# Optimization experiments

Hardware: AMD Instinct MI355X
Metric: run time of the kernel (lower is better)

Reference implementation:

```python
import jax, jax.numpy as jnp
import numpy as np

TEMPERATURE = 0.07
NEG_INF = -9e15
EPS = 1e-12

def setup_inputs() -> dict:
    key = jax.random.key(0)
    k1, k2 = jax.random.split(key)
    N, D = 8192, 128
    features = jax.random.normal(k1, (N, D), dtype=jnp.float32)
    labels = jax.random.randint(k2, (N,), 0, 16, dtype=jnp.int64)
    return {"features": features, "labels": labels}

def reference(features, labels):
    N = features.shape[0]
    # L2 normalize rows (torch F.normalize: x / max(||x||, eps))
    norm = jnp.linalg.norm(features, axis=1, keepdims=True)
    f = features / jnp.maximum(norm, EPS)
    # [N, N] similarity
    sim = jnp.matmul(f, f.T) / TEMPERATURE
    eye = jnp.eye(N, dtype=bool)
    sim = jnp.where(eye, NEG_INF, sim)
    # positive-pair mask: same label, excluding self
    pos_mask = ((labels[:, None] == labels[None, :]) & ~eye).astype(sim.dtype)
    denom = jnp.exp(sim).sum(axis=1, keepdims=True)  # [N, 1]
    log_prob = sim - jnp.log(denom + EPS)
    loss = -(pos_mask * log_prob).sum(axis=1) / (pos_mask.sum(axis=1) + EPS)
    return loss.mean()
```

## Files before the change

kernel.cpp:

```cpp
#include <hip/hip_runtime.h>
#include <hip/hip_bf16.h>

#define EPS 1e-12f
#define SQRT_C_EXP 4.53981597f
#define M_LN2F 0.69314718056f
#define NUM_CLASSES 16

#define BM 256
#define BN 128
#define KD 128
#define NCHUNK 8
#define NPART 16
#define PSTRIDE 48

typedef __attribute__((ext_vector_type(4))) float f32x4;
typedef __attribute__((ext_vector_type(8))) short bf16x8;

__device__ __forceinline__ float bf2f(ushort u) {
    unsigned int x = ((unsigned int)u) << 16;
    return __uint_as_float(x);
}

__device__ __forceinline__ const bf16x8* lds_frag(const ushort* base, int r, int slot) {
    int sw = slot ^ (r & 7);
    return reinterpret_cast<const bf16x8*>(
        reinterpret_cast<const char*>(base) + r * 256 + sw * 16);
}

__global__ void normalize_kernel(const float* __restrict__ feat,
                                 ushort* __restrict__ fb,
                                 float* __restrict__ sq,
                                 int N) {
    int r    = (blockIdx.x * blockDim.x + threadIdx.x) >> 6;
    int lane = threadIdx.x & 63;
    if (r >= N) return;
    const float2 v = *reinterpret_cast<const float2*>(feat + (size_t)r * KD + lane * 2);
    float s = v.x * v.x + v.y * v.y;
    #pragma unroll
    for (int off = 1; off < 64; off <<= 1) s += __shfl_xor(s, off);
    const float scale = SQRT_C_EXP / fmaxf(sqrtf(s), EPS);

    __hip_bfloat16 h0 = __float2bfloat16(v.x * scale);
    __hip_bfloat16 h1 = __float2bfloat16(v.y * scale);
    ushort u0 = *reinterpret_cast<ushort*>(&h0);
    ushort u1 = *reinterpret_cast<ushort*>(&h1);
    unsigned int pack = (unsigned int)u0 | ((unsigned int)u1 << 16);
    *reinterpret_cast<unsigned int*>(fb + (size_t)r * KD + lane * 2) = pack;

    float q0 = bf2f(u0), q1 = bf2f(u1);
    float q = q0 * q0 + q1 * q1;
    #pragma unroll
    for (int off = 1; off < 64; off <<= 1) q += __shfl_xor(q, off);
    if (lane == 0) sq[r] = q;
}

__global__ __launch_bounds__(512, 2) void supcon_denom(
    const ushort* __restrict__ fb,
    const int* __restrict__ labels,
    float* __restrict__ part,
    int N) {

    __shared__ __align__(16) ushort As[BM * KD];
    __shared__ __align__(16) ushort Bs[2][BN * KD];

    const int tid  = threadIdx.x;
    const int lane = tid & 63;
    const int w    = tid >> 6;
    const int wr   = w >> 1;
    const int wc   = w & 1;
    const int r16  = lane & 15;
    const int g4   = lane >> 4;

    const int rowbase = blockIdx.y * BM;
    const int col0    = blockIdx.x * (BN * NCHUNK);

    {
        const ushort* gA = fb + (size_t)rowbase * KD;
        #pragma unroll
        for (int i = 0; i < 8; i++) {
            int c = i * 512 + tid;
            bf16x8 v = *reinterpret_cast<const bf16x8*>(gA + c * 8);
            int dst = c ^ ((c >> 4) & 7);
            *reinterpret_cast<bf16x8*>(&As[dst * 8]) = v;
        }
        const ushort* gB = fb + (size_t)col0 * KD;
        #pragma unroll
        for (int i = 0; i < 4; i++) {
            int c = i * 512 + tid;
            bf16x8 v = *reinterpret_cast<const bf16x8*>(gB + c * 8);
            int dst = c ^ ((c >> 4) & 7);
            *reinterpret_cast<bf16x8*>(&Bs[0][dst * 8]) = v;
        }
    }

    int rlab[4][4];
    #pragma unroll
    for (int m = 0; m < 4; m++)
        #pragma unroll
        for (int i = 0; i < 4; i++)
            rlab[m][i] = labels[rowbase + wr * 64 + m * 16 + g4 * 4 + i];

    __syncthreads();

    bf16x8 a[4][4];
    #pragma unroll
    for (int ks = 0; ks < 4; ks++) {
        const int slot = ks * 4 + g4;
        #pragma unroll
        for (int m = 0; m < 4; m++)
            a[ks][m] = *lds_frag(As, wr * 64 + m * 16 + r16, slot);
    }

    float pd[4][4], pp[4][4], pc[4][4];
    #pragma unroll
    for (int m = 0; m < 4; m++)
        #pragma unroll
        for (int i = 0; i < 4; i++) { pd[m][i] = 0.f; pp[m][i] = 0.f; pc[m][i] = 0.f; }

    int cur = 0;
    for (int c = 0; c < NCHUNK; c++) {
        bf16x8 pre0, pre1, pre2, pre3;
        if (c + 1 < NCHUNK) {
            const ushort* gB = fb + (size_t)(col0 + (c + 1) * BN) * KD;
            pre0 = *reinterpret_cast<const bf16x8*>(gB + (0 * 512 + tid) * 8);
            pre1 = *reinterpret_cast<const bf16x8*>(gB + (1 * 512 + tid) * 8);
            pre2 = *reinterpret_cast<const bf16x8*>(gB + (2 * 512 + tid) * 8);
            pre3 = *reinterpret_cast<const bf16x8*>(gB + (3 * 512 + tid) * 8);
        }
        const int colbase = col0 + c * BN + wc * 64;
        int clab[4];
        #pragma unroll
        for (int n = 0; n < 4; n++)
            clab[n] = labels[colbase + n * 16 + r16];

        f32x4 acc[4][4];
        #pragma unroll
        for (int m = 0; m < 4; m++)
            #pragma unroll
            for (int n = 0; n < 4; n++) acc[m][n] = f32x4{0.f, 0.f, 0.f, 0.f};

        const ushort* bbase = Bs[cur];
        #pragma unroll
        for (int ks = 0; ks < 4; ks++) {
            const int slot = ks * 4 + g4;
            bf16x8 bv[4];
            #pragma unroll
            for (int n = 0; n < 4; n++)
                bv[n] = *lds_frag(bbase, wc * 64 + n * 16 + r16, slot);
            #pragma unroll
            for (int m = 0; m < 4; m++)
                #pragma unroll
                for (int n = 0; n < 4; n++)
                    acc[m][n] = __builtin_amdgcn_mfma_f32_16x16x32_bf16(a[ks][m], bv[n], acc[m][n], 0, 0, 0);
        }

        #pragma unroll
        for (int m = 0; m < 4; m++)
            #pragma unroll
            for (int n = 0; n < 4; n++)
                #pragma unroll
                for (int i = 0; i < 4; i++) {
                    const float sim = acc[m][n][i];
                    pd[m][i] += __builtin_amdgcn_exp2f(sim);
                    const bool mt = (rlab[m][i] == clab[n]);
                    pp[m][i] += mt ? sim : 0.f;
                    pc[m][i] += mt ? 1.f : 0.f;
                }

        if (c + 1 < NCHUNK) {
            ushort* dstb = Bs[cur ^ 1];
            int ch;
            ch = 0 * 512 + tid; *reinterpret_cast<bf16x8*>(&dstb[(ch ^ ((ch >> 4) & 7)) * 8]) = pre0;
            ch = 1 * 512 + tid; *reinterpret_cast<bf16x8*>(&dstb[(ch ^ ((ch >> 4) & 7)) * 8]) = pre1;
            ch = 2 * 512 + tid; *reinterpret_cast<bf16x8*>(&dstb[(ch ^ ((ch >> 4) & 7)) * 8]) = pre2;
            ch = 3 * 512 + tid; *reinterpret_cast<bf16x8*>(&dstb[(ch ^ ((ch >> 4) & 7)) * 8]) = pre3;
        }
        __syncthreads();
        cur ^= 1;
    }

    #pragma unroll
    for (int off = 1; off < 16; off <<= 1)
        #pragma unroll
        for (int m = 0; m < 4; m++)
            #pragma unroll
            for (int i = 0; i < 4; i++) {
                pd[m][i] += __shfl_xor(pd[m][i], off);
                pp[m][i] += __shfl_xor(pp[m][i], off);
                pc[m][i] += __shfl_xor(pc[m][i], off);
            }

    if (r16 == 0) {
        const int slot = blockIdx.x * 2 + wc;
        #pragma unroll
        for (int m = 0; m < 4; m++)
            #pragma unroll
            for (int i = 0; i < 4; i++) {
                int r = rowbase + wr * 64 + m * 16 + g4 * 4 + i;
                float* p = part + (size_t)r * PSTRIDE + slot;
                p[0]  = pd[m][i];
                p[16] = pp[m][i];
                p[32] = pc[m][i];
            }
    }
}

__global__ void rowloss_kernel(const float* __restrict__ part,
                               const float* __restrict__ sq,
                               float* __restrict__ rowloss,
                               int N) {
    int r    = (blockIdx.x * blockDim.x + threadIdx.x) >> 6;
    int lane = threadIdx.x & 63;
    if (r >= N) return;

    float v = (lane < PSTRIDE) ? part[(size_t)r * PSTRIDE + lane] : 0.f;
    #pragma unroll
    for (int off = 1; off < 16; off <<= 1) v += __shfl_xor(v, off);
    float dsum = __shfl(v, 0);
    float psum = __shfl(v, 16);
    float csum = __shfl(v, 32);

    if (lane == 0) {
        float sqr    = sq[r];
        float possum = (psum - sqr) * M_LN2F;
        float cnt    = csum - 1.0f;
        float dn     = dsum - __builtin_amdgcn_exp2f(sqr);
        rowloss[r]   = -(possum - cnt * logf(dn + EPS)) / (cnt + EPS);
    }
}

__global__ void reduce_kernel(const float* __restrict__ rowloss,
                              float* __restrict__ out, int N) {
    __shared__ float sdata[16];
    float s = 0.f;
    for (int r = threadIdx.x; r < N; r += blockDim.x) s += rowloss[r];
    #pragma unroll
    for (int off = 1; off < 64; off <<= 1) s += __shfl_xor(s, off);
    int wv = threadIdx.x >> 6;
    if ((threadIdx.x & 63) == 0) sdata[wv] = s;
    __syncthreads();
    if (threadIdx.x == 0) {
        float t = 0.f;
        int nw = (int)(blockDim.x >> 6);
        for (int i = 0; i < nw; i++) t += sdata[i];
        out[0] = t / (float)N;
    }
}

extern "C" void kernel_launch(void* const* d_in, const int* in_sizes, int n_in,
                              void* d_out, int out_size, void* d_ws, size_t ws_size,
                              hipStream_t stream) {
    const float* feat = (const float*)d_in[0];
    const int* labels = (const int*)d_in[1];
    const int N = in_sizes[1];

    char* ws = (char*)d_ws;
    size_t off = 0;
    ushort* fb     = (ushort*)(ws + off);  off += (size_t)N * KD * sizeof(ushort);
    float* sq      = (float*)(ws + off);   off += (size_t)N * sizeof(float);
    float* part    = (float*)(ws + off);   off += (size_t)N * PSTRIDE * sizeof(float);
    float* rowloss = (float*)(ws + off);

    normalize_kernel<<<(N + 3) / 4, 256, 0, stream>>>(feat, fb, sq, N);

    dim3 grid(N / (BN * NCHUNK), N / BM);
    supcon_denom<<<grid, 512, 0, stream>>>(fb, labels, part, N);

    rowloss_kernel<<<(N + 3) / 4, 256, 0, stream>>>(part, sq, rowloss, N);
    reduce_kernel<<<1, 1024, 0, stream>>>(rowloss, (float*)d_out, N);
}
```

Before: 48.74 us.

## Use direct global-to-LDS loads and process column subtiles sequentially

Replaces the register-staged global loads and LDS stores for the A and B tiles with global_load_lds direct transfers. The swizzle moves from the LDS destination to the global source address. The per-chunk compute is restructured to loop over the four 16-column subtiles one at a time with a 4-accumulator set instead of 16, cutting register pressure. This may raise occupancy, but it serializes MFMA and exp work per subtile, and it relies on the final __syncthreads to wait for the async loads, which is fragile if no explicit vmcnt wait is emitted.

Result: no change. 48.63 us (-0.2%).

```diff
diff --git a/kernel.cpp b/kernel.cpp
--- a/kernel.cpp
+++ b/kernel.cpp
@@ -4,7 +4,6 @@
 #define EPS 1e-12f
 #define SQRT_C_EXP 4.53981597f
 #define M_LN2F 0.69314718056f
-#define NUM_CLASSES 16
 
 #define BM 256
 #define BN 128
@@ -19,6 +18,12 @@
 __device__ __forceinline__ float bf2f(ushort u) {
     unsigned int x = ((unsigned int)u) << 16;
     return __uint_as_float(x);
+}
+
+__device__ __forceinline__ void gload16(const void* g, void* l) {
+    __builtin_amdgcn_global_load_lds(
+        (const __attribute__((address_space(1))) void*)g,
+        (__attribute__((address_space(3))) void*)l, 16, 0, 0);
 }
 
 __device__ __forceinline__ const bf16x8* lds_frag(const ushort* base, int r, int slot) {
@@ -78,18 +83,16 @@
         const ushort* gA = fb + (size_t)rowbase * KD;
         #pragma unroll
         for (int i = 0; i < 8; i++) {
-            int c = i * 512 + tid;
-            bf16x8 v = *reinterpret_cast<const bf16x8*>(gA + c * 8);
-            int dst = c ^ ((c >> 4) & 7);
-            *reinterpret_cast<bf16x8*>(&As[dst * 8]) = v;
+            int d = i * 512 + tid;
+            int s = d ^ ((d >> 4) & 7);
+            gload16(gA + (size_t)s * 8, &As[d * 8]);
         }
         const ushort* gB = fb + (size_t)col0 * KD;
         #pragma unroll
         for (int i = 0; i < 4; i++) {
-            int c = i * 512 + tid;
-            bf16x8 v = *reinterpret_cast<const bf16x8*>(gB + c * 8);
-            int dst = c ^ ((c >> 4) & 7);
-            *reinterpret_cast<bf16x8*>(&Bs[0][dst * 8]) = v;
+            int d = i * 512 + tid;
+            int s = d ^ ((d >> 4) & 7);
+            gload16(gB + (size_t)s * 8, &Bs[0][d * 8]);
         }
     }
 
@@ -119,62 +122,49 @@
 
     int cur = 0;
     for (int c = 0; c < NCHUNK; c++) {
-        bf16x8 pre0, pre1, pre2, pre3;
         if (c + 1 < NCHUNK) {
             const ushort* gB = fb + (size_t)(col0 + (c + 1) * BN) * KD;
-            pre0 = *reinterpret_cast<const bf16x8*>(gB + (0 * 512 + tid) * 8);
-            pre1 = *reinterpret_cast<const bf16x8*>(gB + (1 * 512 + tid) * 8);
-            pre2 = *reinterpret_cast<const bf16x8*>(gB + (2 * 512 + tid) * 8);
-            pre3 = *reinterpret_cast<const bf16x8*>(gB + (3 * 512 + tid) * 8);
-        }
+            ushort* dstb = Bs[cur ^ 1];
+            #pragma unroll
+            for (int i = 0; i < 4; i++) {
+                int d = i * 512 + tid;
+                int s = d ^ ((d >> 4) & 7);
+                gload16(gB + (size_t)s * 8, &dstb[d * 8]);
+            }
+        }
+
+        const ushort* bbase = Bs[cur];
         const int colbase = col0 + c * BN + wc * 64;
-        int clab[4];
-        #pragma unroll
-        for (int n = 0; n < 4; n++)
-            clab[n] = labels[colbase + n * 16 + r16];
-
-        f32x4 acc[4][4];
-        #pragma unroll
-        for (int m = 0; m < 4; m++)
-            #pragma unroll
-            for (int n = 0; n < 4; n++) acc[m][n] = f32x4{0.f, 0.f, 0.f, 0.f};
-
-        const ushort* bbase = Bs[cur];
-        #pragma unroll
-        for (int ks = 0; ks < 4; ks++) {
-            const int slot = ks * 4 + g4;
-            bf16x8 bv[4];
-            #pragma unroll
-            for (int n = 0; n < 4; n++)
-                bv[n] = *lds_frag(bbase, wc * 64 + n * 16 + r16, slot);
+
+        #pragma unroll 1
+        for (int n = 0; n < 4; n++) {
+            const int clab = labels[colbase + n * 16 + r16];
+
+            f32x4 acc[4];
+            #pragma unroll
+            for (int m = 0; m < 4; m++) acc[m] = f32x4{0.f, 0.f, 0.f, 0.f};
+
+            #pragma unroll
+            for (int ks = 0; ks < 4; ks++) {
+                const int slot = ks * 4 + g4;
+                bf16x8 bv = *lds_frag(bbase, wc * 64 + n * 16 + r16, slot);
+                #pragma unroll
+                for (int m = 0; m < 4; m++)
+                    acc[m] = __builtin_amdgcn_mfma_f32_16x16x32_bf16(a[ks][m], bv, acc[m], 0, 0, 0);
+            }
+
             #pragma unroll
             for (int m = 0; m < 4; m++)
                 #pragma unroll
-                for (int n = 0; n < 4; n++)
-                    acc[m][n] = __builtin_amdgcn_mfma_f32_16x16x32_bf16(a[ks][m], bv[n], acc[m][n], 0, 0, 0);
-        }
-
-        #pragma unroll
-        for (int m = 0; m < 4; m++)
-            #pragma unroll
-            for (int n = 0; n < 4; n++)
-                #pragma unroll
                 for (int i = 0; i < 4; i++) {
-                    const float sim = acc[m][n][i];
+                    const float sim = acc[m][i];
                     pd[m][i] += __builtin_amdgcn_exp2f(sim);
-                    const bool mt = (rlab[m][i] == clab[n]);
+                    const bool mt = (rlab[m][i] == clab);
                     pp[m][i] += mt ? sim : 0.f;
                     pc[m][i] += mt ? 1.f : 0.f;
                 }
-
-        if (c + 1 < NCHUNK) {
-            ushort* dstb = Bs[cur ^ 1];
-            int ch;
-            ch = 0 * 512 + tid; *reinterpret_cast<bf16x8*>(&dstb[(ch ^ ((ch >> 4) & 7)) * 8]) = pre0;
-            ch = 1 * 512 + tid; *reinterpret_cast<bf16x8*>(&dstb[(ch ^ ((ch >> 4) & 7)) * 8]) = pre1;
-            ch = 2 * 512 + tid; *reinterpret_cast<bf16x8*>(&dstb[(ch ^ ((ch >> 4) & 7)) * 8]) = pre2;
-            ch = 3 * 512 + tid; *reinterpret_cast<bf16x8*>(&dstb[(ch ^ ((ch >> 4) & 7)) * 8]) = pre3;
-        }
+        }
+
         __syncthreads();
         cur ^= 1;
     }
```
